# Kernel tuning notes

Measured on AMD Instinct MI355X. Metric: run time of the kernel, lower is better.

## Reference

```python
import jax, jax.numpy as jnp
import numpy as np

B, S, D, L = 2, 1024, 1024, 48
K = max(1, int(L * 0.1))  # = 4, matches torch k = max(1, int(num_paths * 0.1))
EPS = 1e-5  # torch LayerNorm default


def setup_inputs() -> dict:
    key = jax.random.key(0)
    ks = jax.random.split(key, 7)
    inv = 1.0 / np.sqrt(D).astype(np.float32)
    return {
        "x": jax.random.normal(ks[0], (B, S, D), jnp.float32),
        "gate_w": jax.random.normal(ks[1], (L, D), jnp.float32) * inv,          # gate_proj weight [L,D], no bias
        "lattice_weights": jax.random.normal(ks[2], (L, D, D), jnp.float32) * 0.02,
        "out_w": jax.random.normal(ks[3], (D, D), jnp.float32) * inv,            # out_proj weight [D,D]
        "out_b": jnp.zeros((D,), jnp.float32),
        "ln_g": jnp.ones((D,), jnp.float32),
        "ln_b": jnp.zeros((D,), jnp.float32),
    }


def reference(x, gate_w, lattice_weights, out_w, out_b, ln_g, ln_b):
    # Gate: top-k routing over L lattice paths
    logits = jnp.einsum('bsd,ld->bsl', x, gate_w)                 # [B,S,L]
    top_vals, idx = jax.lax.top_k(logits, K)                      # [B,S,K] each (descending, like torch.topk)
    scores = jax.nn.softmax(top_vals, axis=-1)                    # [B,S,K]

    # Mathematically identical to gathering [B,S,K,D,D] expert matrices and
    # weight-summing, but computed as one dense GEMM over all L experts
    # followed by a cheap gather -- avoids the 32GB intermediate.
    out_all = jnp.einsum('bsd,lde->bsle', x, lattice_weights)     # [B,S,L,D]
    sel = jnp.take_along_axis(out_all, idx[..., None], axis=2)    # [B,S,K,D]
    lattice_out = jnp.einsum('bskd,bsk->bsd', sel, scores)        # [B,S,D]

    y = x + jnp.einsum('bsd,ed->bse', lattice_out, out_w) + out_b # residual + out_proj
    mu = jnp.mean(y, axis=-1, keepdims=True)
    var = jnp.mean((y - mu) ** 2, axis=-1, keepdims=True)
    return ln_g * (y - mu) * jax.lax.rsqrt(var + EPS) + ln_b
```

## Files before the change

kernel.cpp:

```cpp
#include <hip/hip_runtime.h>
#include <stdint.h>

#define TT 2048
#define DD 1024
#define LL 48
#define SENT (LL * 256)

typedef __attribute__((ext_vector_type(8))) short short8;
typedef __attribute__((ext_vector_type(4))) float f32x4;

static __device__ __forceinline__ unsigned int f2bf(float f) {
  union { float f; unsigned int u; } v; v.f = f;
  return (v.u + 0x7FFFu + ((v.u >> 16) & 1u)) >> 16;
}
static __device__ __forceinline__ unsigned int pack2(float a, float b) {
  return f2bf(a) | (f2bf(b) << 16);
}

#define LGKM0 do { asm volatile("s_waitcnt lgkmcnt(0)" ::: "memory"); \
                   __builtin_amdgcn_sched_barrier(0); } while (0)
#define BAR do { __builtin_amdgcn_s_barrier(); __builtin_amdgcn_sched_barrier(0); } while (0)

__global__ __launch_bounds__(256) void k_gate(
    const float* __restrict__ x, const float* __restrict__ gw,
    unsigned short* __restrict__ xg, int* __restrict__ counts,
    float* __restrict__ bscore, int* __restrict__ tpos)
{
  __shared__ float xs[8][1024];
  __shared__ float lg[8][48];
  __shared__ int tp_s[32];
  const int tid = threadIdx.x;
  const int t0 = blockIdx.x * 8;
  for (int u = tid; u < 2048; u += 256) {
    int tok = u >> 8;
    int c = (u & 255) << 2;
    float4 v = *(const float4*)(x + (size_t)(t0 + tok) * DD + c);
    *(float4*)&xs[tok][c] = v;
  }
  __syncthreads();
  const int lane = tid & 63, wid = tid >> 6;
  for (int li = 0; li < 12; ++li) {
    const int l = wid + (li << 2);
    const float4* gp = (const float4*)(gw + (size_t)l * DD);
    float4 g0 = gp[lane], g1 = gp[lane + 64], g2 = gp[lane + 128], g3 = gp[lane + 192];
    for (int tok = 0; tok < 8; ++tok) {
      const float4* xp = (const float4*)&xs[tok][0];
      float4 a0 = xp[lane], a1 = xp[lane + 64], a2 = xp[lane + 128], a3 = xp[lane + 192];
      float s = a0.x*g0.x + a0.y*g0.y + a0.z*g0.z + a0.w*g0.w
              + a1.x*g1.x + a1.y*g1.y + a1.z*g1.z + a1.w*g1.w
              + a2.x*g2.x + a2.y*g2.y + a2.z*g2.z + a2.w*g2.w
              + a3.x*g3.x + a3.y*g3.y + a3.z*g3.z + a3.w*g3.w;
      #pragma unroll
      for (int off = 32; off; off >>= 1) s += __shfl_down(s, off);
      if (lane == 0) lg[tok][l] = s;
    }
  }
  __syncthreads();
  if (tid < 8) {
    const int tok = tid;
    float v[4]; int id[4];
    unsigned long long taken = 0ull;
    for (int k = 0; k < 4; ++k) {
      float best = -3.4e38f; int bi = 0;
      for (int l = 0; l < 48; ++l) {
        float cand = lg[tok][l];
        if (!((taken >> l) & 1ull) && cand > best) { best = cand; bi = l; }
      }
      taken |= (1ull << bi); v[k] = best; id[k] = bi;
    }
    float e1 = expf(v[1] - v[0]);
    float e2 = expf(v[2] - v[0]);
    float e3 = expf(v[3] - v[0]);
    float inv = 1.0f / (1.0f + e1 + e2 + e3);
    float sc[4] = { inv, e1*inv, e2*inv, e3*inv };
    for (int k = 0; k < 4; ++k) {
      int pos = atomicAdd(&counts[id[k]], 1);
      bscore[id[k] * TT + pos] = sc[k];
      int dst = (pos < 256) ? (id[k] * 256 + pos) : SENT;
      tp_s[tok * 4 + k] = dst;
      tpos[((t0 + tok) << 2) | k] = dst;
    }
  }
  __syncthreads();
  for (int g = 0; g < 32; ++g) {
    int dst = tp_s[g];
    if (dst == SENT) continue;
    const float* src = xs[g >> 2];
    float a0 = src[tid * 4], a1 = src[tid * 4 + 1], a2 = src[tid * 4 + 2], a3 = src[tid * 4 + 3];
    uint2 pk; pk.x = pack2(a0, a1); pk.y = pack2(a2, a3);
    *(uint2*)(xg + (size_t)dst * DD + tid * 4) = pk;
  }
}

__global__ __launch_bounds__(256, 3) void k_expert(
    const unsigned short* __restrict__ xg, const float* __restrict__ W,
    const int* __restrict__ counts, const float* __restrict__ bscore,
    float* __restrict__ selp)
{
  const int l = blockIdx.y;
  const int ncnt = min(counts[l], 256);
  const int n0 = blockIdx.x * 64;
  const int tid = threadIdx.x, lane = tid & 63, wr = tid >> 6;
  const int fr = lane & 15, fq = lane >> 4;

  __shared__ alignas(16) unsigned int Bs[2][16 * 66];
  __shared__ float scs[256];
  scs[tid] = (tid < ncnt) ? bscore[l * TT + tid] : 0.f;

  const unsigned short* ap[4];
  #pragma unroll
  for (int m = 0; m < 4; ++m)
    ap[m] = xg + ((size_t)l << 18) + (size_t)(wr * 64 + m * 16 + fr) * DD + fq * 8;
  const int bp = tid >> 4, e0 = (tid & 15) << 2;
  const float* wsrc0 = W + (size_t)l * DD * DD + (size_t)(bp << 1) * DD + n0 + e0;
  const float* wsrc1 = wsrc0 + DD;

  f32x4 acc[4][4];
  #pragma unroll
  for (int m = 0; m < 4; ++m)
    #pragma unroll
    for (int n = 0; n < 4; ++n)
      #pragma unroll
      for (int j = 0; j < 4; ++j) acc[m][n][j] = 0.f;

  short8 af[2][4];
  float4 rw0[4], rw1[4];

#define E_BLOAD(s, k0) do { \
    rw0[s] = *(const float4*)(wsrc0 + (size_t)(k0) * DD); \
    rw1[s] = *(const float4*)(wsrc1 + (size_t)(k0) * DD); } while (0)
#define E_ALOAD(p, k0) do { \
    af[p][0] = *(const short8*)(ap[0] + (k0)); \
    af[p][1] = *(const short8*)(ap[1] + (k0)); \
    af[p][2] = *(const short8*)(ap[2] + (k0)); \
    af[p][3] = *(const short8*)(ap[3] + (k0)); } while (0)
#define E_BSTORE(buf, s) do { \
    uint4 pv; \
    pv.x = pack2(rw0[s].x, rw1[s].x); pv.y = pack2(rw0[s].y, rw1[s].y); \
    pv.z = pack2(rw0[s].z, rw1[s].z); pv.w = pack2(rw0[s].w, rw1[s].w); \
    *(uint4*)&Bs[buf][bp * 66 + e0] = pv; } while (0)
#define E_COMPUTE(p) do { \
    const unsigned int* Bb = Bs[p]; \
    short8 bf[4]; \
    _Pragma("unroll") for (int n = 0; n < 4; ++n) { \
      const int e = n * 16 + fr; \
      uint4 q; \
      q.x = Bb[(fq * 4 + 0) * 66 + e]; q.y = Bb[(fq * 4 + 1) * 66 + e]; \
      q.z = Bb[(fq * 4 + 2) * 66 + e]; q.w = Bb[(fq * 4 + 3) * 66 + e]; \
      bf[n] = *(short8*)&q; } \
    _Pragma("unroll") for (int m = 0; m < 4; ++m) \
      _Pragma("unroll") for (int n = 0; n < 4; ++n) \
        acc[m][n] = __builtin_amdgcn_mfma_f32_16x16x32_bf16(af[p][m], bf[n], acc[m][n], 0, 0, 0); \
  } while (0)

#define E_BODY(P, PA, SL, SS, T) do { \
    E_BLOAD(SL, (T + 3) * 32); \
    E_ALOAD(PA, (T + 1) * 32); \
    LGKM0; BAR; \
    E_BSTORE(PA, SS); \
    E_COMPUTE(P); } while (0)

  E_BLOAD(0, 0); E_BLOAD(1, 32); E_BLOAD(2, 64);
  E_ALOAD(0, 0);
  E_BSTORE(0, 0);
  for (int t = 0; t < 28; t += 4) {
    E_BODY(0, 1, 3, 1, t + 0);
    E_BODY(1, 0, 0, 2, t + 1);
    E_BODY(0, 1, 1, 3, t + 2);
    E_BODY(1, 0, 2, 0, t + 3);
  }
  E_BODY(0, 1, 3, 1, 28);
  E_ALOAD(0, 30 * 32);
  LGKM0; BAR;
  E_BSTORE(0, 2);
  E_COMPUTE(1);
  E_ALOAD(1, 31 * 32);
  LGKM0; BAR;
  E_BSTORE(1, 3);
  E_COMPUTE(0);
  LGKM0; BAR;
  E_COMPUTE(1);

#undef E_BLOAD
#undef E_ALOAD
#undef E_BSTORE
#undef E_COMPUTE
#undef E_BODY

  #pragma unroll
  for (int m = 0; m < 4; ++m) {
    #pragma unroll
    for (int j = 0; j < 4; ++j) {
      const int r = wr * 64 + m * 16 + fq * 4 + j;
      if (r < ncnt) {
        const float sc = scs[r];
        float* op = selp + (size_t)(l * 256 + r) * DD + n0 + fr;
        #pragma unroll
        for (int n = 0; n < 4; ++n) op[n * 16] = acc[m][n][j] * sc;
      }
    }
  }
}

__global__ __launch_bounds__(256) void k_combine(const float* __restrict__ selp,
    const int* __restrict__ tpos, unsigned short* __restrict__ lat)
{
  const size_t i = ((size_t)blockIdx.x * 256 + threadIdx.x) << 2;
  const size_t t = i >> 10, d = i & 1023;
  int4 tp = *(const int4*)(tpos + (t << 2));
  float4 s0 = *(const float4*)(selp + (size_t)tp.x * DD + d);
  float4 s1 = *(const float4*)(selp + (size_t)tp.y * DD + d);
  float4 s2 = *(const float4*)(selp + (size_t)tp.z * DD + d);
  float4 s3 = *(const float4*)(selp + (size_t)tp.w * DD + d);
  float r0 = s0.x + s1.x + s2.x + s3.x;
  float r1 = s0.y + s1.y + s2.y + s3.y;
  float r2 = s0.z + s1.z + s2.z + s3.z;
  float r3 = s0.w + s1.w + s2.w + s3.w;
  uint2 pk; pk.x = pack2(r0, r1); pk.y = pack2(r2, r3);
  *(uint2*)(lat + i) = pk;
}

__global__ __launch_bounds__(256, 2) void k_outproj(
    const unsigned short* __restrict__ lat, const float* __restrict__ W2,
    const float* __restrict__ xres, const float* __restrict__ bias,
    float* __restrict__ y)
{
  const int n0 = blockIdx.x * 64;
  const int m0 = blockIdx.y * 128;
  const int tid = threadIdx.x, lane = tid & 63, wid = tid >> 6;

  __shared__ alignas(16) unsigned short As[2][128][40];
  __shared__ alignas(16) unsigned short Bs[2][64][40];

  const int aq = tid >> 2, aseg = tid & 3;
  const unsigned short* la0 = lat + (size_t)(m0 + aq) * DD + aseg * 8;
  const unsigned short* la1 = lat + (size_t)(m0 + aq + 64) * DD + aseg * 8;
  const int be = tid >> 2, bks = tid & 3;
  const float* wb = W2 + (size_t)(n0 + be) * DD + bks * 8;

  f32x4 acc[2][4];
  #pragma unroll
  for (int m = 0; m < 2; ++m)
    #pragma unroll
    for (int n = 0; n < 4; ++n)
      #pragma unroll
      for (int j = 0; j < 4; ++j) acc[m][n][j] = 0.f;

  int4 av0, av1;
  float4 w0, w1;

#define O_LOAD(kk) do { \
    av0 = *(const int4*)(la0 + (kk)); \
    av1 = *(const int4*)(la1 + (kk)); \
    w0 = *(const float4*)(wb + (kk)); \
    w1 = *(const float4*)(wb + (kk) + 4); \
  } while (0)

#define O_STORE(b) do { \
    *(int4*)&As[b][aq][aseg * 8]      = av0; \
    *(int4*)&As[b][aq + 64][aseg * 8] = av1; \
    uint4 pv; \
    pv.x = pack2(w0.x, w0.y); pv.y = pack2(w0.z, w0.w); \
    pv.z = pack2(w1.x, w1.y); pv.w = pack2(w1.z, w1.w); \
    *(uint4*)&Bs[b][be][bks * 8] = pv; \
  } while (0)

  O_LOAD(0); O_STORE(0); __syncthreads();
  int cur = 0;
  for (int t = 0; t < 32; ++t) {
    const bool more = (t < 31);
    if (more) O_LOAD((t + 1) * 32);
    short8 af[2], bf[4];
    #pragma unroll
    for (int n = 0; n < 4; ++n)
      bf[n] = *(const short8*)&Bs[cur][n * 16 + (lane & 15)][(lane >> 4) * 8];
    #pragma unroll
    for (int m = 0; m < 2; ++m)
      af[m] = *(const short8*)&As[cur][wid * 32 + m * 16 + (lane & 15)][(lane >> 4) * 8];
    #pragma unroll
    for (int m = 0; m < 2; ++m)
      #pragma unroll
      for (int n = 0; n < 4; ++n)
        acc[m][n] = __builtin_amdgcn_mfma_f32_16x16x32_bf16(af[m], bf[n], acc[m][n], 0, 0, 0);
    if (more) O_STORE(cur ^ 1);
    __syncthreads();
    cur ^= 1;
  }
#undef O_LOAD
#undef O_STORE

  #pragma unroll
  for (int m = 0; m < 2; ++m) {
    #pragma unroll
    for (int j = 0; j < 4; ++j) {
      const int t = m0 + wid * 32 + m * 16 + ((lane >> 4) << 2) + j;
      #pragma unroll
      for (int n = 0; n < 4; ++n) {
        const int e = n0 + n * 16 + (lane & 15);
        y[(size_t)t * DD + e] = xres[(size_t)t * DD + e] + acc[m][n][j] + bias[e];
      }
    }
  }
}

__global__ __launch_bounds__(256) void k_ln(const float* __restrict__ y,
    const float* __restrict__ g, const float* __restrict__ b, float* __restrict__ out)
{
  const int t = blockIdx.x, tid = threadIdx.x;
  float4 v = *(const float4*)(y + (size_t)t * DD + tid * 4);
  float s  = v.x + v.y + v.z + v.w;
  float ss = v.x*v.x + v.y*v.y + v.z*v.z + v.w*v.w;
  #pragma unroll
  for (int off = 32; off; off >>= 1) { s += __shfl_down(s, off); ss += __shfl_down(ss, off); }
  __shared__ float rs[8];
  const int wid = tid >> 6, lane = tid & 63;
  if (lane == 0) { rs[wid] = s; rs[wid + 4] = ss; }
  __syncthreads();
  float S  = rs[0] + rs[1] + rs[2] + rs[3];
  float SS = rs[4] + rs[5] + rs[6] + rs[7];
  float mu = S * (1.0f / DD);
  float var = SS * (1.0f / DD) - mu * mu;
  float inv = rsqrtf(var + 1e-5f);
  float4 gg = *(const float4*)(g + tid * 4);
  float4 bb = *(const float4*)(b + tid * 4);
  float4 o;
  o.x = gg.x * (v.x - mu) * inv + bb.x;
  o.y = gg.y * (v.y - mu) * inv + bb.y;
  o.z = gg.z * (v.z - mu) * inv + bb.z;
  o.w = gg.w * (v.w - mu) * inv + bb.w;
  *(float4*)(out + (size_t)t * DD + tid * 4) = o;
}

extern "C" void kernel_launch(void* const* d_in, const int* in_sizes, int n_in,
                              void* d_out, int out_size, void* d_ws, size_t ws_size,
                              hipStream_t stream) {
  (void)in_sizes; (void)n_in; (void)out_size;
  const float* x   = (const float*)d_in[0];
  const float* gw  = (const float*)d_in[1];
  const float* lw  = (const float*)d_in[2];
  const float* ow  = (const float*)d_in[3];
  const float* obv = (const float*)d_in[4];
  const float* lng = (const float*)d_in[5];
  const float* lnb = (const float*)d_in[6];
  float* out = (float*)d_out;
  char* ws = (char*)d_ws;

  unsigned short* xg     = (unsigned short*)(ws);
  float*          selp   = (float*)(ws + (24ull << 20));
  unsigned short* lat    = (unsigned short*)(ws + (73ull << 20));
  float*          y      = (float*)(ws + (77ull << 20));
  int*            counts = (int*)(ws + (85ull << 20));
  float*          bscore = (float*)(ws + (85ull << 20) + 4096);
  int*            tpos   = (int*)(ws + (86ull << 20));
  if (ws_size < (87ull << 20)) return;

  hipMemsetAsync(counts, 0, LL * sizeof(int), stream);
  hipMemsetAsync(selp + (size_t)SENT * DD, 0, DD * sizeof(float), stream);
  k_gate<<<TT / 8, 256, 0, stream>>>(x, gw, xg, counts, bscore, tpos);
  k_expert<<<dim3(16, LL), 256, 0, stream>>>(xg, lw, counts, bscore, selp);
  k_combine<<<TT * DD / (256 * 4), 256, 0, stream>>>(selp, tpos, lat);
  k_outproj<<<dim3(16, 16), 256, 0, stream>>>(lat, ow, x, obv, y);
  k_ln<<<TT, 256, 0, stream>>>(y, lng, lnb, out);
}
```

Measured before the change: 191.1 us.

## Widen expert GEMM tile to 256x256 with 512-thread blocks and 192-block grid

```diff
diff --git a/kernel.cpp b/kernel.cpp
--- a/kernel.cpp
+++ b/kernel.cpp
@@ -92,100 +92,101 @@
   }
 }
 
-__global__ __launch_bounds__(256, 3) void k_expert(
+__global__ __launch_bounds__(512, 1) void k_expert(
     const unsigned short* __restrict__ xg, const float* __restrict__ W,
     const int* __restrict__ counts, const float* __restrict__ bscore,
     float* __restrict__ selp)
 {
-  const int l = blockIdx.y;
+  const int bid = blockIdx.x;
+  const int l = bid % LL;
+  const int n0 = (bid / LL) * 256;
   const int ncnt = min(counts[l], 256);
-  const int n0 = blockIdx.x * 64;
-  const int tid = threadIdx.x, lane = tid & 63, wr = tid >> 6;
+  const int tid = threadIdx.x, lane = tid & 63, wid = tid >> 6;
+  const int wr = wid & 3, wc = wid >> 2;
   const int fr = lane & 15, fq = lane >> 4;
 
-  __shared__ alignas(16) unsigned int Bs[2][16 * 66];
+  __shared__ alignas(16) unsigned int Bs[2][16 * 264];
   __shared__ float scs[256];
-  scs[tid] = (tid < ncnt) ? bscore[l * TT + tid] : 0.f;
+  if (tid < 256) scs[tid] = (tid < ncnt) ? bscore[l * TT + tid] : 0.f;
 
   const unsigned short* ap[4];
   #pragma unroll
   for (int m = 0; m < 4; ++m)
     ap[m] = xg + ((size_t)l << 18) + (size_t)(wr * 64 + m * 16 + fr) * DD + fq * 8;
-  const int bp = tid >> 4, e0 = (tid & 15) << 2;
+  const int bp = tid >> 5, e0 = (tid & 31) << 3;
   const float* wsrc0 = W + (size_t)l * DD * DD + (size_t)(bp << 1) * DD + n0 + e0;
   const float* wsrc1 = wsrc0 + DD;
 
-  f32x4 acc[4][4];
+  f32x4 acc[4][8];
   #pragma unroll
   for (int m = 0; m < 4; ++m)
     #pragma unroll
-    for (int n = 0; n < 4; ++n)
+    for (int n = 0; n < 8; ++n)
       #pragma unroll
       for (int j = 0; j < 4; ++j) acc[m][n][j] = 0.f;
 
   short8 af[2][4];
-  float4 rw0[4], rw1[4];
+  float4 rw[2][4];
 
 #define E_BLOAD(s, k0) do { \
-    rw0[s] = *(const float4*)(wsrc0 + (size_t)(k0) * DD); \
-    rw1[s] = *(const float4*)(wsrc1 + (size_t)(k0) * DD); } while (0)
+    rw[s][0] = *(const float4*)(wsrc0 + (size_t)(k0) * DD); \
+    rw[s][1] = *(const float4*)(wsrc0 + (size_t)(k0) * DD + 4); \
+    rw[s][2] = *(const float4*)(wsrc1 + (size_t)(k0) * DD); \
+    rw[s][3] = *(const float4*)(wsrc1 + (size_t)(k0) * DD + 4); } while (0)
 #define E_ALOAD(p, k0) do { \
     af[p][0] = *(const short8*)(ap[0] + (k0)); \
     af[p][1] = *(const short8*)(ap[1] + (k0)); \
     af[p][2] = *(const short8*)(ap[2] + (k0)); \
     af[p][3] = *(const short8*)(ap[3] + (k0)); } while (0)
 #define E_BSTORE(buf, s) do { \
-    uint4 pv; \
-    pv.x = pack2(rw0[s].x, rw1[s].x); pv.y = pack2(rw0[s].y, rw1[s].y); \
-    pv.z = pack2(rw0[s].z, rw1[s].z); pv.w = pack2(rw0[s].w, rw1[s].w); \
-    *(uint4*)&Bs[buf][bp * 66 + e0] = pv; } while (0)
-#define E_COMPUTE(p) do { \
-    const unsigned int* Bb = Bs[p]; \
-    short8 bf[4]; \
-    _Pragma("unroll") for (int n = 0; n < 4; ++n) { \
-      const int e = n * 16 + fr; \
+    uint4 p0, p1; \
+    p0.x = pack2(rw[s][0].x, rw[s][2].x); p0.y = pack2(rw[s][0].y, rw[s][2].y); \
+    p0.z = pack2(rw[s][0].z, rw[s][2].z); p0.w = pack2(rw[s][0].w, rw[s][2].w); \
+    p1.x = pack2(rw[s][1].x, rw[s][3].x); p1.y = pack2(rw[s][1].y, rw[s][3].y); \
+    p1.z = pack2(rw[s][1].z, rw[s][3].z); p1.w = pack2(rw[s][1].w, rw[s][3].w); \
+    *(uint4*)&Bs[buf][bp * 264 + e0]     = p0; \
+    *(uint4*)&Bs[buf][bp * 264 + e0 + 4] = p1; } while (0)
+#define E_COMPUTE(buf, p) do { \
+    const unsigned int* Bb = Bs[buf]; \
+    _Pragma("unroll") for (int n = 0; n < 8; ++n) { \
+      const int e = wc * 128 + n * 16 + fr; \
       uint4 q; \
-      q.x = Bb[(fq * 4 + 0) * 66 + e]; q.y = Bb[(fq * 4 + 1) * 66 + e]; \
-      q.z = Bb[(fq * 4 + 2) * 66 + e]; q.w = Bb[(fq * 4 + 3) * 66 + e]; \
-      bf[n] = *(short8*)&q; } \
-    _Pragma("unroll") for (int m = 0; m < 4; ++m) \
-      _Pragma("unroll") for (int n = 0; n < 4; ++n) \
-        acc[m][n] = __builtin_amdgcn_mfma_f32_16x16x32_bf16(af[p][m], bf[n], acc[m][n], 0, 0, 0); \
-  } while (0)
-
-#define E_BODY(P, PA, SL, SS, T) do { \
-    E_BLOAD(SL, (T + 3) * 32); \
-    E_ALOAD(PA, (T + 1) * 32); \
-    LGKM0; BAR; \
-    E_BSTORE(PA, SS); \
-    E_COMPUTE(P); } while (0)
-
-  E_BLOAD(0, 0); E_BLOAD(1, 32); E_BLOAD(2, 64);
+      q.x = Bb[(fq * 4 + 0) * 264 + e]; q.y = Bb[(fq * 4 + 1) * 264 + e]; \
+      q.z = Bb[(fq * 4 + 2) * 264 + e]; q.w = Bb[(fq * 4 + 3) * 264 + e]; \
+      short8 bf = *(short8*)&q; \
+      _Pragma("unroll") for (int m = 0; m < 4; ++m) \
+        acc[m][n] = __builtin_amdgcn_mfma_f32_16x16x32_bf16(af[p][m], bf, acc[m][n], 0, 0, 0); \
+    } } while (0)
+
+  E_BLOAD(0, 0); E_BLOAD(1, 32);
   E_ALOAD(0, 0);
   E_BSTORE(0, 0);
-  for (int t = 0; t < 28; t += 4) {
-    E_BODY(0, 1, 3, 1, t + 0);
-    E_BODY(1, 0, 0, 2, t + 1);
-    E_BODY(0, 1, 1, 3, t + 2);
-    E_BODY(1, 0, 2, 0, t + 3);
-  }
-  E_BODY(0, 1, 3, 1, 28);
-  E_ALOAD(0, 30 * 32);
   LGKM0; BAR;
-  E_BSTORE(0, 2);
-  E_COMPUTE(1);
+  for (int t = 0; t < 30; t += 2) {
+    E_BLOAD(0, (t + 2) * 32);
+    E_ALOAD(1, (t + 1) * 32);
+    E_COMPUTE(0, 0);
+    LGKM0; BAR;
+    E_BSTORE(1, 1);
+    LGKM0; BAR;
+    E_BLOAD(1, (t + 3) * 32);
+    E_ALOAD(0, (t + 2) * 32);
+    E_COMPUTE(1, 1);
+    LGKM0; BAR;
+    E_BSTORE(0, 0);
+    LGKM0; BAR;
+  }
   E_ALOAD(1, 31 * 32);
+  E_COMPUTE(0, 0);
   LGKM0; BAR;
-  E_BSTORE(1, 3);
-  E_COMPUTE(0);
+  E_BSTORE(1, 1);
   LGKM0; BAR;
-  E_COMPUTE(1);
+  E_COMPUTE(1, 1);
 
 #undef E_BLOAD
 #undef E_ALOAD
 #undef E_BSTORE
 #undef E_COMPUTE
-#undef E_BODY
 
   #pragma unroll
   for (int m = 0; m < 4; ++m) {
@@ -194,9 +195,9 @@
       const int r = wr * 64 + m * 16 + fq * 4 + j;
       if (r < ncnt) {
         const float sc = scs[r];
-        float* op = selp + (size_t)(l * 256 + r) * DD + n0 + fr;
+        float* op = selp + (size_t)(l * 256 + r) * DD + n0 + wc * 128 + fr;
         #pragma unroll
-        for (int n = 0; n < 4; ++n) op[n * 16] = acc[m][n][j] * sc;
+        for (int n = 0; n < 8; ++n) op[n * 16] = acc[m][n][j] * sc;
       }
     }
   }
@@ -357,7 +358,7 @@
   hipMemsetAsync(counts, 0, LL * sizeof(int), stream);
   hipMemsetAsync(selp + (size_t)SENT * DD, 0, DD * sizeof(float), stream);
   k_gate<<<TT / 8, 256, 0, stream>>>(x, gw, xg, counts, bscore, tpos);
-  k_expert<<<dim3(16, LL), 256, 0, stream>>>(xg, lw, counts, bscore, selp);
+  k_expert<<<192, 512, 0, stream>>>(xg, lw, counts, bscore, selp);
   k_combine<<<TT * DD / (256 * 4), 256, 0, stream>>>(selp, tpos, lat);
   k_outproj<<<dim3(16, 16), 256, 0, stream>>>(lat, ow, x, obv, y);
   k_ln<<<TT, 256, 0, stream>>>(y, lng, lnb, out);
```

Result: faster. 184.4 us, median of 2 (-3.5%).
